# Kernel optimization log

Hardware: AMD Instinct MI355X
Metric: run time of the kernel (lower is better)

The kernel has to match this reference:

```python
import jax, jax.numpy as jnp
import numpy as np

HEADS = 12
C = 384
FS = 56
WS = 7
WN = FS // WS            # windows per side = 8
NW = WN * WN             # total windows = 64
DISP = WS // 2           # cyclic shift displacement = 3
DK = (C / HEADS) ** (-0.5)


def _create_mask(ws, d, zero_dim=False, one_dim=False):
    m = np.zeros((ws * ws, ws * ws), np.float32)
    if zero_dim:
        m[-d * ws:, :-d * ws] = -np.inf
        m[:-d * ws, -d * ws:] = -np.inf
    if one_dim:
        t = np.zeros((ws, ws), np.float32)
        t[-d:, :-d] = -np.inf
        t[:-d, -d:] = -np.inf
        for i in range(0, ws * ws, ws):
            for j in range(0, ws * ws, ws):
                m[i:i + ws, j:j + ws] = t
    return m


def _window_mask():
    # per-window additive mask [NW, WS*WS, WS*WS] matching the torch slicing
    zm = _create_mask(WS, DISP, zero_dim=True)
    om = _create_mask(WS, DISP, one_dim=True)
    wm = np.zeros((NW, WS * WS, WS * WS), np.float32)
    wm[-WN:] += zm                 # last row of windows
    wm[WN - 1::WN] += om           # last column of windows
    return jnp.asarray(wm)


def _rel_indices():
    idx = np.array([[x, y] for x in range(WS) for y in range(WS)], np.int64)
    rel = idx[None, :, :] - idx[:, None, :] + WS - 1   # [WS^2, WS^2, 2]
    return rel


def _dconv(x, w):
    # depthwise 3x3, padding=1
    return jax.lax.conv_general_dilated(
        x, w, (1, 1), ((1, 1), (1, 1)),
        dimension_numbers=('NCHW', 'OIHW', 'NCHW'),
        feature_group_count=w.shape[0])


def _pconv(x, w, b):
    y = jax.lax.conv_general_dilated(
        x, w, (1, 1), 'VALID', dimension_numbers=('NCHW', 'OIHW', 'NCHW'))
    return y + b[None, :, None, None]


def _to_windows(t):
    # [B, C, H, W] -> [B, heads, NW, WS*WS, head_dim]
    B = t.shape[0]
    hd = C // HEADS
    t = t.reshape(B, HEADS, hd, WN, WS, WN, WS)
    t = t.transpose(0, 1, 3, 5, 4, 6, 2)
    return t.reshape(B, HEADS, NW, WS * WS, hd)


def _from_windows(t):
    # [B, heads, NW, WS*WS, head_dim] -> [B, C, H, W]
    B = t.shape[0]
    hd = C // HEADS
    t = t.reshape(B, HEADS, WN, WN, WS, WS, hd)
    t = t.transpose(0, 1, 6, 2, 4, 3, 5)
    return t.reshape(B, C, FS, FS)


def setup_inputs() -> dict:
    key = jax.random.key(0)
    ks = jax.random.split(key, 8)
    s = 0.05
    return {
        'x': jax.random.normal(ks[0], (16, C, FS, FS), jnp.float32),
        'qkv_dw': jax.random.normal(ks[1], (C, 1, 3, 3), jnp.float32) * s,
        'qkv_pw': jax.random.normal(ks[2], (3 * C, C, 1, 1), jnp.float32) * s,
        'qkv_pb': jax.random.normal(ks[3], (3 * C,), jnp.float32) * s,
        'out_dw': jax.random.normal(ks[4], (C, 1, 3, 3), jnp.float32) * s,
        'out_pw': jax.random.normal(ks[5], (C, C, 1, 1), jnp.float32) * s,
        'out_pb': jax.random.normal(ks[6], (C,), jnp.float32) * s,
        'pos_emb': jax.random.normal(ks[7], (2 * WS - 1, 2 * WS - 1), jnp.float32),
    }


def reference(x, qkv_dw, qkv_pw, qkv_pb, out_dw, out_pw, out_pb, pos_emb):
    rel = _rel_indices()
    wmask = _window_mask()

    x = jnp.roll(x, shift=(-DISP, -DISP), axis=(2, 3))       # cyclic shift
    x = _dconv(x, qkv_dw)
    qkv = _pconv(x, qkv_pw, qkv_pb)
    q, k, v = jnp.split(qkv, 3, axis=1)
    q, k, v = _to_windows(q), _to_windows(k), _to_windows(v)

    dots = jnp.einsum('bhwid,bhwjd->bhwij', q, k) * DK
    bias = pos_emb[rel[:, :, 0], rel[:, :, 1]]               # [WS^2, WS^2]
    dots = dots + bias[None, None, None] + wmask[None, None]

    attn = jax.nn.softmax(dots, axis=-1)
    out = jnp.einsum('bhwij,bhwjd->bhwid', attn, v)
    out = _from_windows(out)

    out = jnp.roll(out, shift=(DISP, DISP), axis=(2, 3))     # cyclic back shift
    out = _dconv(out, out_dw)
    out = _pconv(out, out_pw, out_pb)
    return out
```

## Files before the change

kernel.cpp:

```cpp
#include <hip/hip_runtime.h>
#include <hip/hip_bf16.h>
#include <cstddef>
#include <cstdint>

#define BQ    16
#define CC    384
#define C3    1152
#define HH    56
#define HWP   3136
#define NTOT  (BQ * HWP)
#define NHEAD 12
#define HD    32
#define WSZ   7
#define NWIN  64
#define WSQ   49
#define DKS   0.17677669529663687f
#define DKS2  0.2550347251093104f

typedef __attribute__((ext_vector_type(8))) short bf16x8;
typedef __attribute__((ext_vector_type(4))) float f32x4;

union U128 { uint4 u; bf16x8 v; ushort us[8]; uint ui[4]; };

__device__ __forceinline__ ushort f2b(float f) {
    __hip_bfloat16 h = __float2bfloat16(f);
    return *reinterpret_cast<ushort*>(&h);
}
__device__ __forceinline__ float b2f(ushort u) {
    __hip_bfloat16 h;
    *reinterpret_cast<ushort*>(&h) = u;
    return __bfloat162float(h);
}

__global__ void prep_all(const float* __restrict__ qkv_pw,
                         const float* __restrict__ out_pw,
                         const float* __restrict__ pos,
                         ushort* __restrict__ wA1, ushort* __restrict__ wA2,
                         float* __restrict__ M) {
    const int idx = blockIdx.x * 256 + threadIdx.x;
    if (idx < C3 * CC) {
        wA1[idx] = f2b(qkv_pw[idx]);
    } else if (idx < C3 * CC + CC * CC) {
        const int k = idx - C3 * CC;
        wA2[k] = f2b(out_pw[k]);
    } else {
        const int k = idx - C3 * CC - CC * CC;
        const int v = k >> 12, rem = k & 4095;
        const int j = rem >> 6, i = rem & 63;
        float m = -1e30f;
        if (i < WSQ && j < WSQ) {
            const int pir = i / WSZ, pic = i - pir * WSZ;
            const int pjr = j / WSZ, pjc = j - pjr * WSZ;
            const bool msk = ((v & 2) && ((pir >= 4) != (pjr >= 4))) ||
                             ((v & 1) && ((pic >= 4) != (pjc >= 4)));
            m = msk ? -1e30f : pos[(pjr - pir + 6) * 13 + (pjc - pic + 6)] * 1.4426950408889634f;
        }
        M[k] = m;
    }
}

template <bool BF16IN, int S>
__global__ __launch_bounds__(256) void dconv_px(const void* __restrict__ inv,
                                                const float* __restrict__ dw,
                                                ushort* __restrict__ out) {
    __shared__ ushort pl[6][32][68];
    const int band = blockIdx.x, cg = blockIdx.y, b = blockIdx.z;
    const int i0 = band * 4;
    const int t = threadIdx.x;
    const int ch = t & 31;

    float wreg[9];
    #pragma unroll
    for (int k = 0; k < 9; ++k) wreg[k] = dw[(cg * 32 + ch) * 9 + k];

    if (BF16IN) {
        const ushort* src = (const ushort*)inv;
        const int c8 = t & 3, sc = t >> 2;
        const int cc = sc < 56 ? sc : sc - 56;
        #pragma unroll
        for (int lr = 0; lr < 6; ++lr) {
            const int gi = i0 + lr - 1;
            U128 u; u.u = make_uint4(0, 0, 0, 0);
            if (gi >= 0 && gi < HH) {
                int rr = gi + S; if (rr >= HH) rr -= HH;
                u.u = *(const uint4*)&src[(size_t)(b * HWP + rr * HH + cc) * CC + cg * 32 + c8 * 8];
            }
            #pragma unroll
            for (int k2 = 0; k2 < 8; ++k2) pl[lr][c8 * 8 + k2][sc] = u.us[k2];
        }
    } else {
        const float* src = (const float*)inv;
        const int cq = t & 15, q0 = t >> 4;
        const int scb = cq < 14 ? cq * 4 : cq * 4 - 56;
        #pragma unroll
        for (int k = 0; k < 12; ++k) {
            const int pair = q0 + k * 16;
            const int lc = pair & 31, lr = pair >> 5;
            const int gi = i0 + lr - 1;
            float4 v = make_float4(0.f, 0.f, 0.f, 0.f);
            if (gi >= 0 && gi < HH) {
                int rr = gi + S; if (rr >= HH) rr -= HH;
                v = *(const float4*)&src[((size_t)(b * CC + cg * 32 + lc)) * HWP + rr * HH + scb];
            }
            ushort4 w;
            w.x = f2b(v.x); w.y = f2b(v.y); w.z = f2b(v.z); w.w = f2b(v.w);
            *(ushort4*)&pl[lr][lc][cq * 4] = w;
        }
    }
    __syncthreads();

    const int u = t >> 5;
    #pragma unroll
    for (int iter = 0; iter < 7; ++iter) {
        const int unit = iter * 8 + u;
        const int colb = unit >> 2;
        const int row  = unit & 3;
        const int c0 = colb * 4;
        int sc0 = c0 - 1 + S; if (sc0 >= HH) sc0 -= HH;
        float acc[4] = {0.f, 0.f, 0.f, 0.f};
        #pragma unroll
        for (int di = 0; di < 3; ++di) {
            const ushort* rp = &pl[row + di][ch][0];
            float v[6];
            #pragma unroll
            for (int k = 0; k < 6; ++k) v[k] = b2f(rp[sc0 + k]);
            if (colb == 0)  v[0] = 0.f;
            if (colb == 13) v[5] = 0.f;
            #pragma unroll
            for (int cc2 = 0; cc2 < 4; ++cc2) {
                acc[cc2] += wreg[di * 3 + 0] * v[cc2];
                acc[cc2] += wreg[di * 3 + 1] * v[cc2 + 1];
                acc[cc2] += wreg[di * 3 + 2] * v[cc2 + 2];
            }
        }
        const int orow = i0 + row;
        #pragma unroll
        for (int cc2 = 0; cc2 < 4; ++cc2)
            out[(size_t)(b * HWP + orow * HH + c0 + cc2) * CC + cg * 32 + ch] = f2b(acc[cc2]);
    }
}

template <int OC, bool OUT_BF16>
__global__ __launch_bounds__(256) void pconv_mfma(const ushort* __restrict__ bt,
                                                  const ushort* __restrict__ wa,
                                                  const float* __restrict__ bias,
                                                  void* __restrict__ outv) {
    __shared__ __align__(16) char smem[49152];

    const int nwg = gridDim.x;
    const int cpx = nwg >> 3;
    const int id  = blockIdx.x;
    const int wg  = (id & 7) * cpx + (id >> 3);
    const int oc0 = (wg % (OC / 128)) * 128;
    const int n0  = (wg / (OC / 128)) * 128;

    const int t   = threadIdx.x;
    const int l   = t & 63;
    const int wm  = (t >> 6) >> 1, wn = (t >> 6) & 1;
    const int i15 = l & 15, g = l >> 4;

    f32x4 acc[4][4] = {};

    const int r0 = t >> 2;
    const int kc = ((t & 3) ^ ((t >> 3) & 3)) * 8;
    const size_t gA0 = (size_t)(oc0 + r0) * CC + kc;
    const size_t gA1 = (size_t)(oc0 + r0 + 64) * CC + kc;
    const size_t gB0 = (size_t)(n0 + r0) * CC + kc;
    const size_t gB1 = (size_t)(n0 + r0 + 64) * CC + kc;
    const int ldsOff = (t & 192) * 16;

#define STAGE(buf, k0) do {                                                              \
    char* la_ = smem + (buf) * 16384 + ldsOff;                                           \
    char* lb_ = la_ + 8192;                                                              \
    __builtin_amdgcn_global_load_lds(                                                    \
        (const __attribute__((address_space(1))) void*)(wa + gA0 + (k0)),                \
        (__attribute__((address_space(3))) void*)la_, 16, 0, 0);                         \
    __builtin_amdgcn_global_load_lds(                                                    \
        (const __attribute__((address_space(1))) void*)(wa + gA1 + (k0)),                \
        (__attribute__((address_space(3))) void*)(la_ + 4096), 16, 0, 0);                \
    __builtin_amdgcn_global_load_lds(                                                    \
        (const __attribute__((address_space(1))) void*)(bt + gB0 + (k0)),                \
        (__attribute__((address_space(3))) void*)lb_, 16, 0, 0);                         \
    __builtin_amdgcn_global_load_lds(                                                    \
        (const __attribute__((address_space(1))) void*)(bt + gB1 + (k0)),                \
        (__attribute__((address_space(3))) void*)(lb_ + 4096), 16, 0, 0);                \
} while (0)

    const int colb = (g ^ ((i15 >> 1) & 3)) << 4;
    const int rbA = (wm * 64 + i15) * 64 + colb;
    const int rbB = (wn * 64 + i15) * 64 + colb;

    STAGE(0, 0);
    int slot = 0;
    for (int kt = 0; kt < 12; ++kt) {
        if (kt < 11) {
            const int nslot = (slot == 2) ? 0 : slot + 1;
            STAGE(nslot, (kt + 1) * 32);
            asm volatile("s_waitcnt vmcnt(4)" ::: "memory");
        } else {
            asm volatile("s_waitcnt vmcnt(0)" ::: "memory");
        }
        __builtin_amdgcn_s_barrier();
        const char* bufA = smem + slot * 16384;
        const char* bufB = bufA + 8192;
        bf16x8 a[4], bb[4];
        #pragma unroll
        for (int i = 0; i < 4; ++i) {
            a[i]  = *(const bf16x8*)(bufA + rbA + i * 1024);
            bb[i] = *(const bf16x8*)(bufB + rbB + i * 1024);
        }
        #pragma unroll
        for (int mf = 0; mf < 4; ++mf)
            #pragma unroll
            for (int nf = 0; nf < 4; ++nf)
                acc[mf][nf] = __builtin_amdgcn_mfma_f32_16x16x32_bf16(a[mf], bb[nf], acc[mf][nf], 0, 0, 0);
        slot = (slot == 2) ? 0 : slot + 1;
    }
#undef STAGE

    const int rl = (l >> 4) * 4;
    const int cl = l & 15;
    if (OUT_BF16) {
        __syncthreads();
        ushort (* const sD)[136] = (ushort(*)[136])smem;
        #pragma unroll
        for (int mf = 0; mf < 4; ++mf) {
            const int ocl = wm * 64 + mf * 16 + rl;
            #pragma unroll
            for (int nf = 0; nf < 4; ++nf) {
                const int nl = wn * 64 + nf * 16 + cl;
                ushort4 w4;
                w4.x = f2b(acc[mf][nf][0] + bias[oc0 + ocl + 0]);
                w4.y = f2b(acc[mf][nf][1] + bias[oc0 + ocl + 1]);
                w4.z = f2b(acc[mf][nf][2] + bias[oc0 + ocl + 2]);
                w4.w = f2b(acc[mf][nf][3] + bias[oc0 + ocl + 3]);
                *(ushort4*)&sD[nl][ocl] = w4;
            }
        }
        __syncthreads();
        ushort* outp = (ushort*)outv;
        #pragma unroll
        for (int rr = 0; rr < 8; ++rr) {
            const int r = (t >> 4) + rr * 16;
            const int c8 = (t & 15) * 8;
            *(uint4*)&outp[(size_t)(n0 + r) * C3 + oc0 + c8] = *(const uint4*)&sD[r][c8];
        }
    } else {
        float* outp = (float*)outv;
        #pragma unroll
        for (int mf = 0; mf < 4; ++mf) {
            const int row = oc0 + wm * 64 + mf * 16 + rl;
            #pragma unroll
            for (int r = 0; r < 4; ++r) {
                const float bs = bias[row + r];
                #pragma unroll
                for (int nf = 0; nf < 4; ++nf) {
                    const int n = n0 + wn * 64 + nf * 16 + cl;
                    const int b = n / HWP, p = n - b * HWP;
                    outp[((size_t)b * OC + row + r) * HWP + p] = acc[mf][nf][r] + bs;
                }
            }
        }
    }
}

__global__ __launch_bounds__(64) void attn_mfma(const ushort* __restrict__ qkv,
                                                const float* __restrict__ M,
                                                ushort* __restrict__ out) {
    __shared__ __align__(16) ushort sVw[64 * 40];

    const int w = blockIdx.x, h = blockIdx.y, b = blockIdx.z;
    const int wr = w >> 3, wc = w & 7;
    const int l = threadIdx.x;
    const int i15 = l & 15, g = l >> 4;
    const int hch = h * HD;
    const float* __restrict__ Mv = M + ((((wr == 7) ? 2 : 0) | ((wc == 7) ? 1 : 0)) << 12);

    #pragma unroll
    for (int pass = 0; pass < 4; ++pass) {
        const int e = l + pass * 64;
        const int pix = e >> 2, c8 = e & 3;
        uint4 v = make_uint4(0, 0, 0, 0);
        if (pix < WSQ) {
            const int n = b * HWP + (wr * WSZ + pix / 7) * HH + wc * WSZ + pix % 7;
            v = *(const uint4*)&qkv[(size_t)n * C3 + 2 * CC + hch + c8 * 8];
        }
        const int cst = c8 ^ ((pix >> 2) & 3);
        *(uint4*)&sVw[pix * 40 + cst * 8] = v;
    }

    bf16x8 qf[4], kf[4];
    #pragma unroll
    for (int it = 0; it < 4; ++it) {
        const int i = it * 16 + i15;
        U128 uq, uk;
        uq.u = make_uint4(0, 0, 0, 0);
        uk.u = make_uint4(0, 0, 0, 0);
        if (i < WSQ) {
            const int n = b * HWP + (wr * WSZ + i / 7) * HH + wc * WSZ + i % 7;
            uq.u = *(const uint4*)&qkv[(size_t)n * C3 + hch + g * 8];
            uk.u = *(const uint4*)&qkv[(size_t)n * C3 + CC + hch + g * 8];
        }
        qf[it] = uq.v;
        kf[it] = uk.v;
    }

    f32x4 sS[4][4] = {};
    __builtin_amdgcn_s_setprio(1);
    #pragma unroll
    for (int jt = 0; jt < 4; ++jt)
        #pragma unroll
        for (int it = 0; it < 4; ++it)
            sS[jt][it] = __builtin_amdgcn_mfma_f32_16x16x32_bf16(kf[jt], qf[it], sS[jt][it], 0, 0, 0);
    __builtin_amdgcn_s_setprio(0);

    #pragma unroll
    for (int jt = 0; jt < 4; ++jt) {
        #pragma unroll
        for (int r = 0; r < 4; ++r) {
            const float* mrow = Mv + (jt * 16 + 4 * g + r) * 64 + i15;
            #pragma unroll
            for (int it = 0; it < 4; ++it)
                sS[jt][it][r] = fmaf(sS[jt][it][r], DKS2, mrow[it * 16]);
        }
    }

    #pragma unroll
    for (int it = 0; it < 4; ++it) {
        float sum = 0.f;
        #pragma unroll
        for (int jt = 0; jt < 4; ++jt)
            #pragma unroll
            for (int r = 0; r < 4; ++r) {
                const float e2 = exp2f(sS[jt][it][r]);
                sS[jt][it][r] = e2;
                sum += e2;
            }
        sum += __shfl_xor(sum, 16);
        sum += __shfl_xor(sum, 32);
        const float inv = 1.f / sum;
        #pragma unroll
        for (int jt = 0; jt < 4; ++jt)
            #pragma unroll
            for (int r = 0; r < 4; ++r) sS[jt][it][r] *= inv;
    }

    uint plo[4][4], phi[4][4];
    #pragma unroll
    for (int it = 0; it < 4; ++it)
        #pragma unroll
        for (int jt = 0; jt < 4; ++jt) {
            plo[it][jt] = (uint)f2b(sS[jt][it][0]) | ((uint)f2b(sS[jt][it][1]) << 16);
            phi[it][jt] = (uint)f2b(sS[jt][it][2]) | ((uint)f2b(sS[jt][it][3]) << 16);
        }

    const int srcLo = (2 * (g & 1)) * 16 + i15;
    const int srcHi = srcLo + 16;
    const bool oddHalf = ((g >> 1) & 1) != 0;

    f32x4 oacc[4][2] = {};
    #pragma unroll
    for (int kt = 0; kt < 2; ++kt) {
        bf16x8 bv[2];
        #pragma unroll
        for (int nt = 0; nt < 2; ++nt) {
            U128 u;
            #pragma unroll
            for (int s = 0; s < 8; ++s) {
                const int j = kt * 32 + 8 * g + s;
                const int d = nt * 16 + i15;
                const int cp = (d >> 3) ^ ((j >> 2) & 3);
                u.us[s] = sVw[j * 40 + cp * 8 + (d & 7)];
            }
            bv[nt] = u.v;
        }
        __builtin_amdgcn_s_setprio(1);
        #pragma unroll
        for (int mt = 0; mt < 4; ++mt) {
            U128 pu;
            #pragma unroll
            for (int u2 = 0; u2 < 4; ++u2) {
                const int sl = (u2 >> 1) ? srcHi : srcLo;
                const uint vE = __shfl((u2 & 1) ? phi[mt][2 * kt]     : plo[mt][2 * kt],     sl, 64);
                const uint vO = __shfl((u2 & 1) ? phi[mt][2 * kt + 1] : plo[mt][2 * kt + 1], sl, 64);
                pu.ui[u2] = oddHalf ? vO : vE;
            }
            #pragma unroll
            for (int nt = 0; nt < 2; ++nt)
                oacc[mt][nt] = __builtin_amdgcn_mfma_f32_16x16x32_bf16(pu.v, bv[nt], oacc[mt][nt], 0, 0, 0);
        }
        __builtin_amdgcn_s_setprio(0);
    }

    #pragma unroll
    for (int mt = 0; mt < 4; ++mt)
        #pragma unroll
        for (int nt = 0; nt < 2; ++nt)
            #pragma unroll
            for (int r = 0; r < 4; ++r) {
                const int i = mt * 16 + 4 * g + r;
                const int d = nt * 16 + i15;
                const int cp = (d >> 3) ^ ((i >> 2) & 3);
                sVw[i * 40 + cp * 8 + (d & 7)] = f2b(oacc[mt][nt][r]);
            }

    #pragma unroll
    for (int pass = 0; pass < 4; ++pass) {
        const int e = l + pass * 64;
        const int pix = e >> 2, c8 = e & 3;
        if (pix < WSQ) {
            const int n = b * HWP + (wr * WSZ + pix / 7) * HH + wc * WSZ + pix % 7;
            const int cp = c8 ^ ((pix >> 2) & 3);
            *(uint4*)&out[(size_t)n * CC + hch + c8 * 8] = *(const uint4*)&sVw[pix * 40 + cp * 8];
        }
    }
}

extern "C" void kernel_launch(void* const* d_in, const int* in_sizes, int n_in,
                              void* d_out, int out_size, void* d_ws, size_t ws_size,
                              hipStream_t stream) {
    const float* x      = (const float*)d_in[0];
    const float* qkv_dw = (const float*)d_in[1];
    const float* qkv_pw = (const float*)d_in[2];
    const float* qkv_pb = (const float*)d_in[3];
    const float* out_dw = (const float*)d_in[4];
    const float* out_pw = (const float*)d_in[5];
    const float* out_pb = (const float*)d_in[6];
    const float* pos    = (const float*)d_in[7];

    ushort* A   = (ushort*)d_ws;
    ushort* B   = A + (size_t)NTOT * CC;
    ushort* wA1 = B + (size_t)NTOT * C3;
    ushort* wA2 = wA1 + (size_t)C3 * CC;
    float*  Mw  = (float*)(wA2 + (size_t)CC * CC);

    prep_all<<<2368, 256, 0, stream>>>(qkv_pw, out_pw, pos, wA1, wA2, Mw);

    dconv_px<false, 3><<<dim3(14, 12, BQ), 256, 0, stream>>>(x, qkv_dw, A);
    pconv_mfma<C3, true><<<dim3((C3 / 128) * (NTOT / 128)), 256, 0, stream>>>(A, wA1, qkv_pb, B);
    attn_mfma<<<dim3(NWIN, NHEAD, BQ), 64, 0, stream>>>(B, Mw, A);
    dconv_px<true, 53><<<dim3(14, 12, BQ), 256, 0, stream>>>(A, out_dw, B);
    pconv_mfma<CC, false><<<dim3((CC / 128) * (NTOT / 128)), 256, 0, stream>>>(B, wA2, out_pb, (float*)d_out);
}
```

Measured before the change: 192.9 us.

## Use 128x256 tiles with 512 threads and double buffering for QKV pointwise GEMM

Splits the templated pointwise-conv GEMM into two kernels. The QKV projection now uses 8 waves per block computing a 128x256 output tile, double-buffered LDS staging instead of triple, and an XCD-aware block remap that handles non-multiple-of-8 grids. The wider tile reuses each weight tile across more pixels to cut global/LDS traffic. In exchange it adds an extra barrier per k-step and a two-pass epilogue, and may lower occupancy.

```diff
diff --git a/kernel.cpp b/kernel.cpp
--- a/kernel.cpp
+++ b/kernel.cpp
@@ -140,19 +140,127 @@
     }
 }
 
-template <int OC, bool OUT_BF16>
-__global__ __launch_bounds__(256) void pconv_mfma(const ushort* __restrict__ bt,
-                                                  const ushort* __restrict__ wa,
-                                                  const float* __restrict__ bias,
-                                                  void* __restrict__ outv) {
+__global__ __launch_bounds__(512) void pconv1_mfma(const ushort* __restrict__ bt,
+                                                   const ushort* __restrict__ wa,
+                                                   const float* __restrict__ bias,
+                                                   ushort* __restrict__ outp) {
+    __shared__ __align__(16) char smem[49152];
+
+    const int nwg = gridDim.x;
+    const int q8 = nwg >> 3, r8 = nwg & 7;
+    const int id = blockIdx.x;
+    const int xcd = id & 7, off = id >> 3;
+    const int wg = (xcd < r8 ? xcd * (q8 + 1) : r8 * (q8 + 1) + (xcd - r8) * q8) + off;
+    const int oc0 = (wg % 9) * 128;
+    const int n0  = (wg / 9) * 256;
+
+    const int t   = threadIdx.x;
+    const int l   = t & 63;
+    const int w   = t >> 6;
+    const int wm  = w >> 2, wn = w & 3;
+    const int i15 = l & 15, g = l >> 4;
+
+    f32x4 acc[4][4] = {};
+
+    const int kc = ((t & 3) ^ ((t >> 3) & 3)) * 8;
+    const size_t gA0 = (size_t)(oc0 + (t >> 2)) * CC + kc;
+    const size_t gB0 = (size_t)(n0 + (t >> 2)) * CC + kc;
+    const size_t gB1 = (size_t)(n0 + (t >> 2) + 128) * CC + kc;
+    const int ldsOff = w * 1024;
+
+#define STAGE(buf, k0) do {                                                              \
+    char* ba_ = smem + (buf) * 24576;                                                    \
+    __builtin_amdgcn_global_load_lds(                                                    \
+        (const __attribute__((address_space(1))) void*)(wa + gA0 + (k0)),                \
+        (__attribute__((address_space(3))) void*)(ba_ + ldsOff), 16, 0, 0);              \
+    __builtin_amdgcn_global_load_lds(                                                    \
+        (const __attribute__((address_space(1))) void*)(bt + gB0 + (k0)),                \
+        (__attribute__((address_space(3))) void*)(ba_ + 8192 + ldsOff), 16, 0, 0);       \
+    __builtin_amdgcn_global_load_lds(                                                    \
+        (const __attribute__((address_space(1))) void*)(bt + gB1 + (k0)),                \
+        (__attribute__((address_space(3))) void*)(ba_ + 16384 + ldsOff), 16, 0, 0);      \
+} while (0)
+
+    const int colb = (g ^ ((i15 >> 1) & 3)) << 4;
+    const int rbA = (wm * 64 + i15) * 64 + colb;
+    const int rbB = (wn * 64 + i15) * 64 + colb;
+
+    STAGE(0, 0);
+    int cur = 0;
+    for (int kt = 0; kt < 12; ++kt) {
+        if (kt < 11) {
+            STAGE(cur ^ 1, (kt + 1) * 32);
+            asm volatile("s_waitcnt vmcnt(3)" ::: "memory");
+        } else {
+            asm volatile("s_waitcnt vmcnt(0)" ::: "memory");
+        }
+        __builtin_amdgcn_s_barrier();
+        const char* bufA = smem + cur * 24576;
+        const char* bufB = bufA + 8192;
+        bf16x8 a[4], bb[4];
+        #pragma unroll
+        for (int i = 0; i < 4; ++i) {
+            a[i]  = *(const bf16x8*)(bufA + rbA + i * 1024);
+            bb[i] = *(const bf16x8*)(bufB + rbB + i * 1024);
+        }
+        #pragma unroll
+        for (int mf = 0; mf < 4; ++mf)
+            #pragma unroll
+            for (int nf = 0; nf < 4; ++nf)
+                acc[mf][nf] = __builtin_amdgcn_mfma_f32_16x16x32_bf16(a[mf], bb[nf], acc[mf][nf], 0, 0, 0);
+        __builtin_amdgcn_sched_barrier(0);
+        __builtin_amdgcn_s_barrier();
+        cur ^= 1;
+    }
+#undef STAGE
+
+    const int rl = (l >> 4) * 4;
+    const int cl = l & 15;
+    ushort (* const sD)[136] = (ushort(*)[136])smem;
+
+    __syncthreads();
+    #pragma unroll
+    for (int p = 0; p < 2; ++p) {
+        if ((wn >> 1) == p) {
+            #pragma unroll
+            for (int mf = 0; mf < 4; ++mf) {
+                const int ocl = wm * 64 + mf * 16 + rl;
+                #pragma unroll
+                for (int nf = 0; nf < 4; ++nf) {
+                    const int nl = (wn & 1) * 64 + nf * 16 + cl;
+                    ushort4 w4;
+                    w4.x = f2b(acc[mf][nf][0] + bias[oc0 + ocl + 0]);
+                    w4.y = f2b(acc[mf][nf][1] + bias[oc0 + ocl + 1]);
+                    w4.z = f2b(acc[mf][nf][2] + bias[oc0 + ocl + 2]);
+                    w4.w = f2b(acc[mf][nf][3] + bias[oc0 + ocl + 3]);
+                    *(ushort4*)&sD[nl][ocl] = w4;
+                }
+            }
+        }
+        __syncthreads();
+        #pragma unroll
+        for (int rr = 0; rr < 4; ++rr) {
+            const int r = (t >> 4) + rr * 32;
+            const int c8 = (t & 15) * 8;
+            *(uint4*)&outp[(size_t)(n0 + p * 128 + r) * C3 + oc0 + c8] =
+                *(const uint4*)&sD[r][c8];
+        }
+        __syncthreads();
+    }
+}
+
+__global__ __launch_bounds__(256) void pconv2_mfma(const ushort* __restrict__ bt,
+                                                   const ushort* __restrict__ wa,
+                                                   const float* __restrict__ bias,
+                                                   float* __restrict__ outp) {
     __shared__ __align__(16) char smem[49152];
 
     const int nwg = gridDim.x;
     const int cpx = nwg >> 3;
     const int id  = blockIdx.x;
     const int wg  = (id & 7) * cpx + (id >> 3);
-    const int oc0 = (wg % (OC / 128)) * 128;
-    const int n0  = (wg / (OC / 128)) * 128;
+    const int oc0 = (wg % (CC / 128)) * 128;
+    const int n0  = (wg / (CC / 128)) * 128;
 
     const int t   = threadIdx.x;
     const int l   = t & 63;
@@ -220,45 +328,17 @@
 
     const int rl = (l >> 4) * 4;
     const int cl = l & 15;
-    if (OUT_BF16) {
-        __syncthreads();
-        ushort (* const sD)[136] = (ushort(*)[136])smem;
-        #pragma unroll
-        for (int mf = 0; mf < 4; ++mf) {
-            const int ocl = wm * 64 + mf * 16 + rl;
+    #pragma unroll
+    for (int mf = 0; mf < 4; ++mf) {
+        const int row = oc0 + wm * 64 + mf * 16 + rl;
+        #pragma unroll
+        for (int r = 0; r < 4; ++r) {
+            const float bs = bias[row + r];
             #pragma unroll
             for (int nf = 0; nf < 4; ++nf) {
-                const int nl = wn * 64 + nf * 16 + cl;
-                ushort4 w4;
-                w4.x = f2b(acc[mf][nf][0] + bias[oc0 + ocl + 0]);
-                w4.y = f2b(acc[mf][nf][1] + bias[oc0 + ocl + 1]);
-                w4.z = f2b(acc[mf][nf][2] + bias[oc0 + ocl + 2]);
-                w4.w = f2b(acc[mf][nf][3] + bias[oc0 + ocl + 3]);
-                *(ushort4*)&sD[nl][ocl] = w4;
-            }
-        }
-        __syncthreads();
-        ushort* outp = (ushort*)outv;
-        #pragma unroll
-        for (int rr = 0; rr < 8; ++rr) {
-            const int r = (t >> 4) + rr * 16;
-            const int c8 = (t & 15) * 8;
-            *(uint4*)&outp[(size_t)(n0 + r) * C3 + oc0 + c8] = *(const uint4*)&sD[r][c8];
-        }
-    } else {
-        float* outp = (float*)outv;
-        #pragma unroll
-        for (int mf = 0; mf < 4; ++mf) {
-            const int row = oc0 + wm * 64 + mf * 16 + rl;
-            #pragma unroll
-            for (int r = 0; r < 4; ++r) {
-                const float bs = bias[row + r];
-                #pragma unroll
-                for (int nf = 0; nf < 4; ++nf) {
-                    const int n = n0 + wn * 64 + nf * 16 + cl;
-                    const int b = n / HWP, p = n - b * HWP;
-                    outp[((size_t)b * OC + row + r) * HWP + p] = acc[mf][nf][r] + bs;
-                }
+                const int n = n0 + wn * 64 + nf * 16 + cl;
+                const int b = n / HWP, p = n - b * HWP;
+                outp[((size_t)b * CC + row + r) * HWP + p] = acc[mf][nf][r] + bs;
             }
         }
     }
@@ -437,8 +517,8 @@
     prep_all<<<2368, 256, 0, stream>>>(qkv_pw, out_pw, pos, wA1, wA2, Mw);
 
     dconv_px<false, 3><<<dim3(14, 12, BQ), 256, 0, stream>>>(x, qkv_dw, A);
-    pconv_mfma<C3, true><<<dim3((C3 / 128) * (NTOT / 128)), 256, 0, stream>>>(A, wA1, qkv_pb, B);
+    pconv1_mfma<<<dim3(9 * (NTOT / 256)), 512, 0, stream>>>(A, wA1, qkv_pb, B);
     attn_mfma<<<dim3(NWIN, NHEAD, BQ), 64, 0, stream>>>(B, Mw, A);
     dconv_px<true, 53><<<dim3(14, 12, BQ), 256, 0, stream>>>(A, out_dw, B);
-    pconv_mfma<CC, false><<<dim3((CC / 128) * (NTOT / 128)), 256, 0, stream>>>(B, wA2, out_pb, (float*)d_out);
-}
+    pconv2_mfma<<<dim3((CC / 128) * (NTOT / 128)), 256, 0, stream>>>(B, wA2, out_pb, (float*)d_out);
+}
```

Result: slower. 204.0 us (+5.7%).
